# Optimization experiments

Measured on AMD Instinct MI355X. Metric: run time of the kernel, lower is better.

Reference implementation:

```python
import jax, jax.numpy as jnp
import numpy as np

N = 50000        # nodes
E = 800000       # edges
MUL = 32         # multiplicity per irrep (32x0e + 32x1o)
NSPEC = 4        # atom species (node_attrs one-hot width)
NBESSEL = 8      # edge_embedding basis size
HID = 8          # invariant_neurons
WNUM = 4 * MUL   # tp.weight_numel (4 'uvu' paths x 32)


def setup_inputs() -> dict:
    key = jax.random.key(0)
    ks = jax.random.split(key, 13)
    return {
        "edge_embedding": jax.random.normal(ks[0], (E, NBESSEL), jnp.float32),
        "node_attrs": jax.random.uniform(ks[1], (N, NSPEC), jnp.float32),
        "node_features": jax.random.normal(ks[2], (N, MUL * 4), jnp.float32),
        "edge_index": jax.random.randint(ks[3], (2, E), 0, N, jnp.int64),
        "edge_attrs": jax.random.normal(ks[4], (E, 4), jnp.float32),
        # linear_1 (per-irrep channel mixing)
        "W1_s": jax.random.normal(ks[5], (MUL, MUL), jnp.float32),
        "W1_v": jax.random.normal(ks[6], (MUL, MUL), jnp.float32),
        # fc: [8] -> [8] -> [128]
        "Wfc1": jax.random.normal(ks[7], (NBESSEL, HID), jnp.float32),
        "Wfc2": jax.random.normal(ks[8], (HID, WNUM), jnp.float32),
        # linear_2: 64x0e+64x1o -> 32x0e+32x1o
        "W2_s": jax.random.normal(ks[9], (2 * MUL, MUL), jnp.float32),
        "W2_v": jax.random.normal(ks[10], (2 * MUL, MUL), jnp.float32),
        # sc: FullyConnectedTensorProduct(32x0e+32x1o, 4x0e -> 32x0e+32x1o)
        "Wsc_s": jax.random.normal(ks[11], (MUL, NSPEC, MUL), jnp.float32),
        "Wsc_v": jax.random.normal(ks[12], (MUL, NSPEC, MUL), jnp.float32),
    }


def reference(edge_embedding, node_attrs, node_features, edge_index, edge_attrs,
              W1_s, W1_v, Wfc1, Wfc2, W2_s, W2_v, Wsc_s, Wsc_v):
    s = node_features[:, :MUL]                       # [N,32] 0e
    v = node_features[:, MUL:].reshape(N, MUL, 3)    # [N,32,3] 1o

    # self-connection: FullyConnectedTensorProduct(features, node_attrs)
    inv = 1.0 / np.sqrt(MUL * NSPEC).astype(np.float32)
    sc_s = jnp.einsum('nu,nz,uzv->nv', s, node_attrs, Wsc_s) * inv
    sc_v = jnp.einsum('nui,nz,uzv->nvi', v, node_attrs, Wsc_v) * inv

    # linear_1 (equivariant: mixes channels within each irrep)
    lin = np.float32(1.0 / np.sqrt(MUL))
    s1 = (s @ W1_s) * lin
    v1 = jnp.einsum('nui,uv->nvi', v, W1_v) * lin

    # fc MLP on edge_embedding -> per-edge TP weights [E,128]
    h = jax.nn.silu((edge_embedding @ Wfc1) * np.float32(1.0 / np.sqrt(NBESSEL)))
    w = (h @ Wfc2) * np.float32(1.0 / np.sqrt(HID))
    w0, w1, w2, w3 = w[:, :MUL], w[:, MUL:2*MUL], w[:, 2*MUL:3*MUL], w[:, 3*MUL:]

    ctr, nbr = edge_index[0], edge_index[1]
    xs = s1[nbr]            # [E,32] gathered scalars
    xv = v1[nbr]            # [E,32,3] gathered vectors
    es = edge_attrs[:, :1]  # [E,1]  edge 0e
    ev = edge_attrs[:, 1:4] # [E,3]  edge 1o

    # weighted CG tensor product ('uvu', per-edge weights)
    out_s0 = w0 * xs * es                                              # 0e x 0e -> 0e
    out_s3 = w3 * jnp.einsum('eui,ei->eu', xv, ev) * np.float32(1/np.sqrt(3))  # 1o x 1o -> 0e
    out_v1 = (w1 * xs)[:, :, None] * ev[:, None, :]                    # 0e x 1o -> 1o
    out_v2 = (w2 * es)[:, :, None] * xv                                # 1o x 0e -> 1o

    e_s = jnp.concatenate([out_s0, out_s3], axis=1)    # [E,64]
    e_v = jnp.concatenate([out_v1, out_v2], axis=1)    # [E,64,3]

    # scatter-sum back to center nodes
    n_s = jax.ops.segment_sum(e_s, ctr, num_segments=N)
    n_v = jax.ops.segment_sum(e_v.reshape(E, -1), ctr, num_segments=N).reshape(N, 2*MUL, 3)

    # linear_2 + residual self-connection
    lin2 = np.float32(1.0 / np.sqrt(2 * MUL))
    out_s = (n_s @ W2_s) * lin2 + sc_s
    out_v = jnp.einsum('nui,uv->nvi', n_v, W2_v) * lin2 + sc_v

    return jnp.concatenate([out_s, out_v.reshape(N, MUL * 3)], axis=1)
```

## Files before the change

### kernel.cpp

```cpp
#include <hip/hip_runtime.h>

#define N_NODES 50000
#define E_EDGES 800000
#define MUL 32
#define CAP 48

typedef _Float16 half2v __attribute__((ext_vector_type(2)));

__device__ __forceinline__ unsigned bfpack2(float a, float b) {
    unsigned ua = __float_as_uint(a), ub = __float_as_uint(b);
    ua = (ua + 0x7FFFu + ((ua >> 16) & 1u)) >> 16;
    ub = (ub + 0x7FFFu + ((ub >> 16) & 1u)) >> 16;
    return ua | (ub << 16);
}
__device__ __forceinline__ float bflo(unsigned p) { return __uint_as_float(p << 16); }
__device__ __forceinline__ float bfhi(unsigned p) { return __uint_as_float(p & 0xFFFF0000u); }
__device__ __forceinline__ unsigned pkh2(float a, float b) {
    union { _Float16 h[2]; unsigned u; } x;
    x.h[0] = (_Float16)a; x.h[1] = (_Float16)b; return x.u;
}
__device__ __forceinline__ half2v ashalf2(unsigned u) {
    union { unsigned u; half2v h; } x; x.u = u; return x.h;
}

__global__ __launch_bounds__(512) void node_pre_sc(
    const float* __restrict__ nf, const float* __restrict__ attrs,
    const float* __restrict__ W1s, const float* __restrict__ W1v,
    const float* __restrict__ Wscs, const float* __restrict__ Wscv,
    uint2* __restrict__ xq, float* __restrict__ out, int* __restrict__ cnt)
{
    for (int i = blockIdx.x * 512 + threadIdx.x; i < N_NODES; i += gridDim.x * 512)
        cnt[i] = 0;

    __shared__ float sW1s[1024];
    __shared__ float sW1v[1024];
    __shared__ float sWscsT[4096];
    __shared__ float sWscvT[4096];
    __shared__ float snf[16][128];
    for (int i = threadIdx.x; i < 1024; i += 512) { sW1s[i] = W1s[i]; sW1v[i] = W1v[i]; }
    for (int i = threadIdx.x; i < 4096; i += 512) {
        int u = i >> 7, rem = i & 127, z = rem >> 5, vv = rem & 31;
        int t = ((u * 32 + vv) << 2) + z;
        sWscsT[t] = Wscs[i];
        sWscvT[t] = Wscv[i];
    }
    __syncthreads();
    int g = threadIdx.x >> 5, v = threadIdx.x & 31;
    int lane = threadIdx.x & 63;
    int wbase = (threadIdx.x >> 6) * 2;
    int sg = wbase + (lane >> 5);
    const float lin = 0.17677669529663687f;
    const float inv = 0.08838834764831845f;
    const float4* nf4 = (const float4*)nf;
    const float4* at4 = (const float4*)attrs;
    for (int node0 = blockIdx.x * 16; node0 < N_NODES; node0 += gridDim.x * 16) {
        {
            int nn = node0 + sg;
            float4 ld = (nn < N_NODES) ? nf4[(long long)nn * 32 + (lane & 31)]
                                       : make_float4(0.f, 0.f, 0.f, 0.f);
            *(float4*)&snf[sg][(lane & 31) * 4] = ld;
        }
        int n = node0 + g;
        if (n >= N_NODES) continue;
        float4 az = at4[n];
        float acc_s = 0.f, a0 = 0.f, a1 = 0.f, a2 = 0.f;
        float scs = 0.f, scv0 = 0.f, scv1 = 0.f, scv2 = 0.f;
#pragma unroll
        for (int u = 0; u < 32; ++u) {
            float su = snf[g][u];
            float x0 = snf[g][32 + u * 3 + 0];
            float x1 = snf[g][32 + u * 3 + 1];
            float x2 = snf[g][32 + u * 3 + 2];
            acc_s += su * sW1s[u * 32 + v];
            float wv = sW1v[u * 32 + v];
            a0 += x0 * wv; a1 += x1 * wv; a2 += x2 * wv;
            int t = (u * 32 + v) << 2;
            float4 cs4 = *(const float4*)&sWscsT[t];
            float4 cv4 = *(const float4*)&sWscvT[t];
            float cs = az.x * cs4.x + az.y * cs4.y + az.z * cs4.z + az.w * cs4.w;
            scs += su * cs;
            float cv = az.x * cv4.x + az.y * cv4.y + az.z * cv4.z + az.w * cv4.w;
            scv0 += x0 * cv; scv1 += x1 * cv; scv2 += x2 * cv;
        }
        uint2 q;
        q.x = bfpack2(acc_s * lin, a0 * lin);
        q.y = bfpack2(a1 * lin, a2 * lin);
        xq[n * 32 + v] = q;
        long long ob = (long long)n * 128;
        out[ob + v] = scs * inv;
        out[ob + 32 + v * 3 + 0] = scv0 * inv;
        out[ob + 32 + v * 3 + 1] = scv1 * inv;
        out[ob + 32 + v * 3 + 2] = scv2 * inv;
    }
}

__global__ __launch_bounds__(256) void edge_prep(
    const float* __restrict__ ee, const float* __restrict__ Wfc1,
    const int* __restrict__ ei, const float* __restrict__ ea,
    int* __restrict__ cnt, int* __restrict__ nbrl, uint4* __restrict__ rec)
{
    __shared__ float sW[64];
    if (threadIdx.x < 64) sW[threadIdx.x] = Wfc1[threadIdx.x];
    __syncthreads();
    long long e = (long long)blockIdx.x * 256 + threadIdx.x;
    if (e >= E_EDGES) return;

    int c = ei[e];
    int nbr = ei[E_EDGES + e];
    int slot = atomicAdd(&cnt[c], 1);

    const float4* p = (const float4*)(ee + e * 8);
    float4 a = p[0], b = p[1];
    float emb[8] = {a.x, a.y, a.z, a.w, b.x, b.y, b.z, b.w};
    const float sfc = 0.35355339059327373f;
    float h[8];
#pragma unroll
    for (int k = 0; k < 8; ++k) {
        float acc = 0.f;
#pragma unroll
        for (int t = 0; t < 8; ++t) acc += emb[t] * sW[t * 8 + k];
        acc *= sfc;
        h[k] = acc / (1.f + __expf(-acc));
    }
    float4 av = ((const float4*)ea)[e];

    if (slot < CAP) {
        int idx = c * CAP + slot;
        nbrl[idx] = nbr;
        uint4 A;
        A.x = pkh2(h[0], h[1]); A.y = pkh2(h[2], h[3]);
        A.z = pkh2(h[4], h[5]); A.w = pkh2(h[6], h[7]);
        uint2 C;
        C.x = bfpack2(av.x, av.y); C.y = bfpack2(av.z, av.w);
        rec[(long long)idx * 2] = A;
        *(uint2*)(rec + (long long)idx * 2 + 1) = C;
    }
}

__global__ __launch_bounds__(256, 6) void gather(
    const int* __restrict__ cnt, const int* __restrict__ nbrl,
    const uint4* __restrict__ rec,
    const uint2* __restrict__ xq, const float* __restrict__ Wfc2,
    float4* __restrict__ m4)
{
    int wid = threadIdx.x >> 6;
    int lane = threadIdx.x & 63;
    int u = lane & 31;
    int half = lane >> 5;
    const float sfc = 0.35355339059327373f;
    const float is3 = 0.5773502691896258f;
    half2v wf0[4], wf1[4], wf2[4], wf3[4];
#pragma unroll
    for (int t = 0; t < 4; ++t) {
        wf0[t] = half2v{(_Float16)(Wfc2[(2*t) * 128 + u] * sfc),
                        (_Float16)(Wfc2[(2*t+1) * 128 + u] * sfc)};
        wf1[t] = half2v{(_Float16)(Wfc2[(2*t) * 128 + 32 + u] * sfc),
                        (_Float16)(Wfc2[(2*t+1) * 128 + 32 + u] * sfc)};
        wf2[t] = half2v{(_Float16)(Wfc2[(2*t) * 128 + 64 + u] * sfc),
                        (_Float16)(Wfc2[(2*t+1) * 128 + 64 + u] * sfc)};
        wf3[t] = half2v{(_Float16)(Wfc2[(2*t) * 128 + 96 + u] * (sfc * is3)),
                        (_Float16)(Wfc2[(2*t+1) * 128 + 96 + u] * (sfc * is3))};
    }
    for (int n = blockIdx.x * 4 + wid; n < N_NODES; n += gridDim.x * 4) {
        int deg = cnt[n];
        if (deg > CAP) deg = CAP;
        int T = (deg + 1) >> 1;
        long long base = (long long)n * CAP;
        int nbr_all = (lane < deg) ? nbrl[base + lane] : 0;
        float as0 = 0.f, as3 = 0.f;
        float av10 = 0.f, av11 = 0.f, av12 = 0.f;
        float av20 = 0.f, av21 = 0.f, av22 = 0.f;
        uint4 A_c = {0, 0, 0, 0};
        uint2 C_c = {0, 0}, q_c = {0, 0};
        float m_c = 0.f;
        if (T > 0) {
            int j = half;
            m_c = (j < deg) ? 1.f : 0.f;
            int js = (j < deg) ? j : 0;
            int nbr = __shfl(nbr_all, js);
            A_c = rec[(base + js) * 2];
            C_c = *(const uint2*)(rec + (base + js) * 2 + 1);
            q_c = xq[nbr * 32 + u];
        }
        for (int t = 0; t < T; ++t) {
            uint4 A_n = {0, 0, 0, 0};
            uint2 C_n = {0, 0}, q_n = {0, 0};
            float m_n = 0.f;
            if (t + 1 < T) {
                int j = 2 * (t + 1) + half;
                m_n = (j < deg) ? 1.f : 0.f;
                int js = (j < deg) ? j : 0;
                int nbr = __shfl(nbr_all, js);
                A_n = rec[(base + js) * 2];
                C_n = *(const uint2*)(rec + (base + js) * 2 + 1);
                q_n = xq[nbr * 32 + u];
            }
            half2v h01 = ashalf2(A_c.x), h23 = ashalf2(A_c.y);
            half2v h45 = ashalf2(A_c.z), h67 = ashalf2(A_c.w);
            float w0 = 0.f, w1 = 0.f, w2 = 0.f, w3 = 0.f;
            w0 = __builtin_amdgcn_fdot2(h01, wf0[0], w0, false);
            w1 = __builtin_amdgcn_fdot2(h01, wf1[0], w1, false);
            w2 = __builtin_amdgcn_fdot2(h01, wf2[0], w2, false);
            w3 = __builtin_amdgcn_fdot2(h01, wf3[0], w3, false);
            w0 = __builtin_amdgcn_fdot2(h23, wf0[1], w0, false);
            w1 = __builtin_amdgcn_fdot2(h23, wf1[1], w1, false);
            w2 = __builtin_amdgcn_fdot2(h23, wf2[1], w2, false);
            w3 = __builtin_amdgcn_fdot2(h23, wf3[1], w3, false);
            w0 = __builtin_amdgcn_fdot2(h45, wf0[2], w0, false);
            w1 = __builtin_amdgcn_fdot2(h45, wf1[2], w1, false);
            w2 = __builtin_amdgcn_fdot2(h45, wf2[2], w2, false);
            w3 = __builtin_amdgcn_fdot2(h45, wf3[2], w3, false);
            w0 = __builtin_amdgcn_fdot2(h67, wf0[3], w0, false);
            w1 = __builtin_amdgcn_fdot2(h67, wf1[3], w1, false);
            w2 = __builtin_amdgcn_fdot2(h67, wf2[3], w2, false);
            w3 = __builtin_amdgcn_fdot2(h67, wf3[3], w3, false);
            w0 *= m_c; w1 *= m_c; w2 *= m_c; w3 *= m_c;
            float es  = bflo(C_c.x), ev0 = bfhi(C_c.x);
            float ev1 = bflo(C_c.y), ev2 = bfhi(C_c.y);
            float xs  = bflo(q_c.x), xv0 = bfhi(q_c.x);
            float xv1 = bflo(q_c.y), xv2 = bfhi(q_c.y);
            as0 += w0 * xs * es;
            as3 += w3 * (xv0 * ev0 + xv1 * ev1 + xv2 * ev2);
            float t1 = w1 * xs;
            float t2 = w2 * es;
            av10 += t1 * ev0; av11 += t1 * ev1; av12 += t1 * ev2;
            av20 += t2 * xv0; av21 += t2 * xv1; av22 += t2 * xv2;
            A_c = A_n; C_c = C_n; q_c = q_n; m_c = m_n;
        }
        as0  += __shfl_xor(as0, 32);
        as3  += __shfl_xor(as3, 32);
        av10 += __shfl_xor(av10, 32);
        av11 += __shfl_xor(av11, 32);
        av12 += __shfl_xor(av12, 32);
        av20 += __shfl_xor(av20, 32);
        av21 += __shfl_xor(av21, 32);
        av22 += __shfl_xor(av22, 32);
        if (half == 0) m4[(long long)n * 64 + u]      = make_float4(av10, av11, av12, as0);
        else           m4[(long long)n * 64 + 32 + u] = make_float4(av20, av21, av22, as3);
    }
}

__global__ __launch_bounds__(512) void node_post(
    const float4* __restrict__ m4,
    const float* __restrict__ W2s, const float* __restrict__ W2v,
    float* __restrict__ out)
{
    __shared__ float sW2s[2048];
    __shared__ float sW2v[2048];
    __shared__ float4 sm[16][64];
    for (int i = threadIdx.x; i < 2048; i += 512) { sW2s[i] = W2s[i]; sW2v[i] = W2v[i]; }
    __syncthreads();
    int g = threadIdx.x >> 5, v = threadIdx.x & 31;
    int lane = threadIdx.x & 63;
    int sg = (threadIdx.x >> 6) * 2 + (lane >> 5);
    const float lin2 = 0.125f;
    for (int node0 = blockIdx.x * 16; node0 < N_NODES; node0 += gridDim.x * 16) {
        {
            int nn = node0 + sg;
            int s0 = (lane & 31) * 2;
            float4 z = make_float4(0.f, 0.f, 0.f, 0.f);
            float4 a = (nn < N_NODES) ? m4[(long long)nn * 64 + s0] : z;
            float4 b = (nn < N_NODES) ? m4[(long long)nn * 64 + s0 + 1] : z;
            sm[sg][s0] = a;
            sm[sg][s0 + 1] = b;
        }
        int n = node0 + g;
        if (n >= N_NODES) continue;
        float os = 0.f, ov0 = 0.f, ov1 = 0.f, ov2 = 0.f;
#pragma unroll 16
        for (int U = 0; U < 64; ++U) {
            float4 q = sm[g][U];
            os += q.w * sW2s[U * 32 + v];
            float wv = sW2v[U * 32 + v];
            ov0 += q.x * wv; ov1 += q.y * wv; ov2 += q.z * wv;
        }
        long long ob = (long long)n * 128;
        out[ob + v] += os * lin2;
        out[ob + 32 + v * 3 + 0] += ov0 * lin2;
        out[ob + 32 + v * 3 + 1] += ov1 * lin2;
        out[ob + 32 + v * 3 + 2] += ov2 * lin2;
    }
}

extern "C" void kernel_launch(void* const* d_in, const int* in_sizes, int n_in,
                              void* d_out, int out_size, void* d_ws, size_t ws_size,
                              hipStream_t stream) {
    const float* ee    = (const float*)d_in[0];
    const float* attrs = (const float*)d_in[1];
    const float* nf    = (const float*)d_in[2];
    const int*   ei    = (const int*)d_in[3];
    const float* ea    = (const float*)d_in[4];
    const float* W1s   = (const float*)d_in[5];
    const float* W1v   = (const float*)d_in[6];
    const float* Wfc1  = (const float*)d_in[7];
    const float* Wfc2  = (const float*)d_in[8];
    const float* W2s   = (const float*)d_in[9];
    const float* W2v   = (const float*)d_in[10];
    const float* Wscs  = (const float*)d_in[11];
    const float* Wscv  = (const float*)d_in[12];
    float* out = (float*)d_out;

    uint2*  xq   = (uint2*)d_ws;
    uint4*  rec  = (uint4*)(xq + (size_t)N_NODES * 32);
    float4* m4   = (float4*)(rec + (size_t)N_NODES * CAP * 2);
    int*    cnt  = (int*)(m4 + (size_t)N_NODES * 64);
    int*    nbrl = cnt + N_NODES;

    node_pre_sc<<<768, 512, 0, stream>>>(nf, attrs, W1s, W1v, Wscs, Wscv, xq, out, cnt);
    edge_prep<<<(E_EDGES + 255) / 256, 256, 0, stream>>>(ee, Wfc1, ei, ea, cnt, nbrl, rec);
    gather<<<2048, 256, 0, stream>>>(cnt, nbrl, rec, xq, Wfc2, m4);
    node_post<<<1024, 512, 0, stream>>>(m4, W2s, W2v, out);
}
```

Measured before the change: 350.5 us.

## Fuse node and edge prep kernels, store gather output as bf16

Merges the node pre-processing and edge preparation kernels into one launch whose blocks are split by blockIdx into node-work and edge-work roles, so the two independent stages can run concurrently. The counter reset moves to a hipMemsetAsync, which is needed because edge blocks now run alongside node blocks and could no longer rely on the node kernel zeroing the counters. The gather output is packed to bf16, halving its write and read traffic, and node_post now reads it directly from global memory instead of staging it through shared memory. The bf16 intermediate lowers the precision of the aggregated messages.

```diff
diff --git a/kernel.cpp b/kernel.cpp
--- a/kernel.cpp
+++ b/kernel.cpp
@@ -23,117 +23,120 @@
     union { unsigned u; half2v h; } x; x.u = u; return x.h;
 }
 
-__global__ __launch_bounds__(512) void node_pre_sc(
+#define NODE_BLOCKS 768
+#define EDGE_BLOCKS 1024
+#define PREP_GRID (NODE_BLOCKS + EDGE_BLOCKS)
+
+__global__ __launch_bounds__(512) void prep(
     const float* __restrict__ nf, const float* __restrict__ attrs,
     const float* __restrict__ W1s, const float* __restrict__ W1v,
     const float* __restrict__ Wscs, const float* __restrict__ Wscv,
-    uint2* __restrict__ xq, float* __restrict__ out, int* __restrict__ cnt)
+    const float* __restrict__ ee, const float* __restrict__ Wfc1,
+    const int* __restrict__ ei, const float* __restrict__ ea,
+    uint2* __restrict__ xq, float* __restrict__ out,
+    int* __restrict__ cnt, int* __restrict__ nbrl, uint4* __restrict__ rec)
 {
-    for (int i = blockIdx.x * 512 + threadIdx.x; i < N_NODES; i += gridDim.x * 512)
-        cnt[i] = 0;
-
     __shared__ float sW1s[1024];
     __shared__ float sW1v[1024];
     __shared__ float sWscsT[4096];
     __shared__ float sWscvT[4096];
     __shared__ float snf[16][128];
-    for (int i = threadIdx.x; i < 1024; i += 512) { sW1s[i] = W1s[i]; sW1v[i] = W1v[i]; }
-    for (int i = threadIdx.x; i < 4096; i += 512) {
-        int u = i >> 7, rem = i & 127, z = rem >> 5, vv = rem & 31;
-        int t = ((u * 32 + vv) << 2) + z;
-        sWscsT[t] = Wscs[i];
-        sWscvT[t] = Wscv[i];
-    }
-    __syncthreads();
-    int g = threadIdx.x >> 5, v = threadIdx.x & 31;
-    int lane = threadIdx.x & 63;
-    int wbase = (threadIdx.x >> 6) * 2;
-    int sg = wbase + (lane >> 5);
-    const float lin = 0.17677669529663687f;
-    const float inv = 0.08838834764831845f;
-    const float4* nf4 = (const float4*)nf;
-    const float4* at4 = (const float4*)attrs;
-    for (int node0 = blockIdx.x * 16; node0 < N_NODES; node0 += gridDim.x * 16) {
-        {
-            int nn = node0 + sg;
-            float4 ld = (nn < N_NODES) ? nf4[(long long)nn * 32 + (lane & 31)]
-                                       : make_float4(0.f, 0.f, 0.f, 0.f);
-            *(float4*)&snf[sg][(lane & 31) * 4] = ld;
-        }
-        int n = node0 + g;
-        if (n >= N_NODES) continue;
-        float4 az = at4[n];
-        float acc_s = 0.f, a0 = 0.f, a1 = 0.f, a2 = 0.f;
-        float scs = 0.f, scv0 = 0.f, scv1 = 0.f, scv2 = 0.f;
+    __shared__ float sWfc[64];
+
+    int m7 = blockIdx.x % 7;
+    if (m7 < 3) {
+        int nb = (blockIdx.x / 7) * 3 + m7;
+        for (int i = threadIdx.x; i < 1024; i += 512) { sW1s[i] = W1s[i]; sW1v[i] = W1v[i]; }
+        for (int i = threadIdx.x; i < 4096; i += 512) {
+            int u = i >> 7, rem = i & 127, z = rem >> 5, vv = rem & 31;
+            int t = ((u * 32 + vv) << 2) + z;
+            sWscsT[t] = Wscs[i];
+            sWscvT[t] = Wscv[i];
+        }
+        __syncthreads();
+        int g = threadIdx.x >> 5, v = threadIdx.x & 31;
+        int lane = threadIdx.x & 63;
+        int sg = (threadIdx.x >> 6) * 2 + (lane >> 5);
+        const float lin = 0.17677669529663687f;
+        const float inv = 0.08838834764831845f;
+        const float4* nf4 = (const float4*)nf;
+        const float4* at4 = (const float4*)attrs;
+        for (int node0 = nb * 16; node0 < N_NODES; node0 += NODE_BLOCKS * 16) {
+            {
+                int nn = node0 + sg;
+                float4 ld = (nn < N_NODES) ? nf4[(long long)nn * 32 + (lane & 31)]
+                                           : make_float4(0.f, 0.f, 0.f, 0.f);
+                *(float4*)&snf[sg][(lane & 31) * 4] = ld;
+            }
+            int n = node0 + g;
+            if (n >= N_NODES) continue;
+            float4 az = at4[n];
+            float acc_s = 0.f, a0 = 0.f, a1 = 0.f, a2 = 0.f;
+            float scs = 0.f, scv0 = 0.f, scv1 = 0.f, scv2 = 0.f;
 #pragma unroll
-        for (int u = 0; u < 32; ++u) {
-            float su = snf[g][u];
-            float x0 = snf[g][32 + u * 3 + 0];
-            float x1 = snf[g][32 + u * 3 + 1];
-            float x2 = snf[g][32 + u * 3 + 2];
-            acc_s += su * sW1s[u * 32 + v];
-            float wv = sW1v[u * 32 + v];
-            a0 += x0 * wv; a1 += x1 * wv; a2 += x2 * wv;
-            int t = (u * 32 + v) << 2;
-            float4 cs4 = *(const float4*)&sWscsT[t];
-            float4 cv4 = *(const float4*)&sWscvT[t];
-            float cs = az.x * cs4.x + az.y * cs4.y + az.z * cs4.z + az.w * cs4.w;
-            scs += su * cs;
-            float cv = az.x * cv4.x + az.y * cv4.y + az.z * cv4.z + az.w * cv4.w;
-            scv0 += x0 * cv; scv1 += x1 * cv; scv2 += x2 * cv;
-        }
-        uint2 q;
-        q.x = bfpack2(acc_s * lin, a0 * lin);
-        q.y = bfpack2(a1 * lin, a2 * lin);
-        xq[n * 32 + v] = q;
-        long long ob = (long long)n * 128;
-        out[ob + v] = scs * inv;
-        out[ob + 32 + v * 3 + 0] = scv0 * inv;
-        out[ob + 32 + v * 3 + 1] = scv1 * inv;
-        out[ob + 32 + v * 3 + 2] = scv2 * inv;
-    }
-}
-
-__global__ __launch_bounds__(256) void edge_prep(
-    const float* __restrict__ ee, const float* __restrict__ Wfc1,
-    const int* __restrict__ ei, const float* __restrict__ ea,
-    int* __restrict__ cnt, int* __restrict__ nbrl, uint4* __restrict__ rec)
-{
-    __shared__ float sW[64];
-    if (threadIdx.x < 64) sW[threadIdx.x] = Wfc1[threadIdx.x];
-    __syncthreads();
-    long long e = (long long)blockIdx.x * 256 + threadIdx.x;
-    if (e >= E_EDGES) return;
-
-    int c = ei[e];
-    int nbr = ei[E_EDGES + e];
-    int slot = atomicAdd(&cnt[c], 1);
-
-    const float4* p = (const float4*)(ee + e * 8);
-    float4 a = p[0], b = p[1];
-    float emb[8] = {a.x, a.y, a.z, a.w, b.x, b.y, b.z, b.w};
-    const float sfc = 0.35355339059327373f;
-    float h[8];
+            for (int u = 0; u < 32; ++u) {
+                float su = snf[g][u];
+                float x0 = snf[g][32 + u * 3 + 0];
+                float x1 = snf[g][32 + u * 3 + 1];
+                float x2 = snf[g][32 + u * 3 + 2];
+                acc_s += su * sW1s[u * 32 + v];
+                float wv = sW1v[u * 32 + v];
+                a0 += x0 * wv; a1 += x1 * wv; a2 += x2 * wv;
+                int t = (u * 32 + v) << 2;
+                float4 cs4 = *(const float4*)&sWscsT[t];
+                float4 cv4 = *(const float4*)&sWscvT[t];
+                float cs = az.x * cs4.x + az.y * cs4.y + az.z * cs4.z + az.w * cs4.w;
+                scs += su * cs;
+                float cv = az.x * cv4.x + az.y * cv4.y + az.z * cv4.z + az.w * cv4.w;
+                scv0 += x0 * cv; scv1 += x1 * cv; scv2 += x2 * cv;
+            }
+            uint2 q;
+            q.x = bfpack2(acc_s * lin, a0 * lin);
+            q.y = bfpack2(a1 * lin, a2 * lin);
+            xq[n * 32 + v] = q;
+            long long ob = (long long)n * 128;
+            out[ob + v] = scs * inv;
+            out[ob + 32 + v * 3 + 0] = scv0 * inv;
+            out[ob + 32 + v * 3 + 1] = scv1 * inv;
+            out[ob + 32 + v * 3 + 2] = scv2 * inv;
+        }
+    } else {
+        int eb = (blockIdx.x / 7) * 4 + (m7 - 3);
+        if (threadIdx.x < 64) sWfc[threadIdx.x] = Wfc1[threadIdx.x];
+        __syncthreads();
+        const float sfc = 0.35355339059327373f;
+        for (long long e = (long long)eb * 512 + threadIdx.x; e < E_EDGES;
+             e += (long long)EDGE_BLOCKS * 512) {
+            int c = ei[e];
+            int nbr = ei[E_EDGES + e];
+            int slot = atomicAdd(&cnt[c], 1);
+
+            const float4* p = (const float4*)(ee + e * 8);
+            float4 a = p[0], b = p[1];
+            float emb[8] = {a.x, a.y, a.z, a.w, b.x, b.y, b.z, b.w};
+            float h[8];
 #pragma unroll
-    for (int k = 0; k < 8; ++k) {
-        float acc = 0.f;
+            for (int k = 0; k < 8; ++k) {
+                float acc = 0.f;
 #pragma unroll
-        for (int t = 0; t < 8; ++t) acc += emb[t] * sW[t * 8 + k];
-        acc *= sfc;
-        h[k] = acc / (1.f + __expf(-acc));
-    }
-    float4 av = ((const float4*)ea)[e];
-
-    if (slot < CAP) {
-        int idx = c * CAP + slot;
-        nbrl[idx] = nbr;
-        uint4 A;
-        A.x = pkh2(h[0], h[1]); A.y = pkh2(h[2], h[3]);
-        A.z = pkh2(h[4], h[5]); A.w = pkh2(h[6], h[7]);
-        uint2 C;
-        C.x = bfpack2(av.x, av.y); C.y = bfpack2(av.z, av.w);
-        rec[(long long)idx * 2] = A;
-        *(uint2*)(rec + (long long)idx * 2 + 1) = C;
+                for (int t = 0; t < 8; ++t) acc += emb[t] * sWfc[t * 8 + k];
+                acc *= sfc;
+                h[k] = acc / (1.f + __expf(-acc));
+            }
+            float4 av = ((const float4*)ea)[e];
+
+            if (slot < CAP) {
+                int idx = c * CAP + slot;
+                nbrl[idx] = nbr;
+                uint4 A;
+                A.x = pkh2(h[0], h[1]); A.y = pkh2(h[2], h[3]);
+                A.z = pkh2(h[4], h[5]); A.w = pkh2(h[6], h[7]);
+                uint2 C;
+                C.x = bfpack2(av.x, av.y); C.y = bfpack2(av.z, av.w);
+                rec[(long long)idx * 2] = A;
+                *(uint2*)(rec + (long long)idx * 2 + 1) = C;
+            }
+        }
     }
 }
 
@@ -141,7 +144,7 @@
     const int* __restrict__ cnt, const int* __restrict__ nbrl,
     const uint4* __restrict__ rec,
     const uint2* __restrict__ xq, const float* __restrict__ Wfc2,
-    float4* __restrict__ m4)
+    uint2* __restrict__ m2)
 {
     int wid = threadIdx.x >> 6;
     int lane = threadIdx.x & 63;
@@ -235,44 +238,41 @@
         av20 += __shfl_xor(av20, 32);
         av21 += __shfl_xor(av21, 32);
         av22 += __shfl_xor(av22, 32);
-        if (half == 0) m4[(long long)n * 64 + u]      = make_float4(av10, av11, av12, as0);
-        else           m4[(long long)n * 64 + 32 + u] = make_float4(av20, av21, av22, as3);
+        uint2 o;
+        if (half == 0) {
+            o.x = bfpack2(av10, av11); o.y = bfpack2(av12, as0);
+            m2[(long long)n * 64 + u] = o;
+        } else {
+            o.x = bfpack2(av20, av21); o.y = bfpack2(av22, as3);
+            m2[(long long)n * 64 + 32 + u] = o;
+        }
     }
 }
 
 __global__ __launch_bounds__(512) void node_post(
-    const float4* __restrict__ m4,
+    const uint2* __restrict__ m2,
     const float* __restrict__ W2s, const float* __restrict__ W2v,
     float* __restrict__ out)
 {
     __shared__ float sW2s[2048];
     __shared__ float sW2v[2048];
-    __shared__ float4 sm[16][64];
     for (int i = threadIdx.x; i < 2048; i += 512) { sW2s[i] = W2s[i]; sW2v[i] = W2v[i]; }
     __syncthreads();
     int g = threadIdx.x >> 5, v = threadIdx.x & 31;
-    int lane = threadIdx.x & 63;
-    int sg = (threadIdx.x >> 6) * 2 + (lane >> 5);
     const float lin2 = 0.125f;
     for (int node0 = blockIdx.x * 16; node0 < N_NODES; node0 += gridDim.x * 16) {
-        {
-            int nn = node0 + sg;
-            int s0 = (lane & 31) * 2;
-            float4 z = make_float4(0.f, 0.f, 0.f, 0.f);
-            float4 a = (nn < N_NODES) ? m4[(long long)nn * 64 + s0] : z;
-            float4 b = (nn < N_NODES) ? m4[(long long)nn * 64 + s0 + 1] : z;
-            sm[sg][s0] = a;
-            sm[sg][s0 + 1] = b;
-        }
         int n = node0 + g;
         if (n >= N_NODES) continue;
+        const uint2* mp = m2 + (long long)n * 64;
         float os = 0.f, ov0 = 0.f, ov1 = 0.f, ov2 = 0.f;
-#pragma unroll 16
+#pragma unroll 8
         for (int U = 0; U < 64; ++U) {
-            float4 q = sm[g][U];
-            os += q.w * sW2s[U * 32 + v];
+            uint2 q = mp[U];
+            float v0 = bflo(q.x), v1 = bfhi(q.x);
+            float v2 = bflo(q.y), s = bfhi(q.y);
+            os += s * sW2s[U * 32 + v];
             float wv = sW2v[U * 32 + v];
-            ov0 += q.x * wv; ov1 += q.y * wv; ov2 += q.z * wv;
+            ov0 += v0 * wv; ov1 += v1 * wv; ov2 += v2 * wv;
         }
         long long ob = (long long)n * 128;
         out[ob + v] += os * lin2;
@@ -302,12 +302,13 @@
 
     uint2*  xq   = (uint2*)d_ws;
     uint4*  rec  = (uint4*)(xq + (size_t)N_NODES * 32);
-    float4* m4   = (float4*)(rec + (size_t)N_NODES * CAP * 2);
-    int*    cnt  = (int*)(m4 + (size_t)N_NODES * 64);
+    uint2*  m2   = (uint2*)(rec + (size_t)N_NODES * CAP * 2);
+    int*    cnt  = (int*)(m2 + (size_t)N_NODES * 64);
     int*    nbrl = cnt + N_NODES;
 
-    node_pre_sc<<<768, 512, 0, stream>>>(nf, attrs, W1s, W1v, Wscs, Wscv, xq, out, cnt);
-    edge_prep<<<(E_EDGES + 255) / 256, 256, 0, stream>>>(ee, Wfc1, ei, ea, cnt, nbrl, rec);
-    gather<<<2048, 256, 0, stream>>>(cnt, nbrl, rec, xq, Wfc2, m4);
-    node_post<<<1024, 512, 0, stream>>>(m4, W2s, W2v, out);
-}
+    hipMemsetAsync(cnt, 0, (size_t)N_NODES * sizeof(int), stream);
+    prep<<<PREP_GRID, 512, 0, stream>>>(nf, attrs, W1s, W1v, Wscs, Wscv,
+                                        ee, Wfc1, ei, ea, xq, out, cnt, nbrl, rec);
+    gather<<<2048, 256, 0, stream>>>(cnt, nbrl, rec, xq, Wfc2, m2);
+    node_post<<<1024, 512, 0, stream>>>(m2, W2s, W2v, out);
+}
```

Result: no change. 355.7 us (+1.5%).
